# Optimization experiments

Measured on AMD Instinct MI355X. Metric: run time of the kernel, lower is better.

## Reference

```python
import jax, jax.numpy as jnp
import numpy as np

N_SRC = 50000
N_DST = 50000
N_EDGES = 1_600_000
D_IN = 128
D_OUT = 128
NUM_HEADS = 8
SCALE = float((D_OUT // NUM_HEADS) ** 0.5)


def setup_inputs() -> dict:
    key = jax.random.key(0)
    ks = jax.random.split(key, 10)
    s = 1.0 / np.sqrt(D_IN)
    return {
        "src_feat": jax.random.normal(ks[0], (N_SRC, D_IN), dtype=jnp.float32),
        "dst_feat": jax.random.normal(ks[1], (N_DST, D_OUT), dtype=jnp.float32),
        "src_idx": jax.random.randint(ks[2], (N_EDGES,), 0, N_SRC, dtype=jnp.int64),
        "dst_idx": jax.random.randint(ks[3], (N_EDGES,), 0, N_DST, dtype=jnp.int64),
        "Wq": jax.random.normal(ks[4], (D_OUT, D_OUT), dtype=jnp.float32) * s,
        "bq": jnp.zeros((D_OUT,), dtype=jnp.float32),
        "Wk": jax.random.normal(ks[5], (D_OUT, D_IN), dtype=jnp.float32) * s,
        "bk": jnp.zeros((D_OUT,), dtype=jnp.float32),
        "Wv": jax.random.normal(ks[6], (D_OUT, D_IN), dtype=jnp.float32) * s,
        "bv": jnp.zeros((D_OUT,), dtype=jnp.float32),
    }


def reference(src_feat, dst_feat, src_idx, dst_idx, Wq, bq, Wk, bk, Wv, bv):
    # Node-level projections (torch Linear: x @ W.T + b)
    Q = dst_feat @ Wq.T + bq            # [N_dst, D_OUT]
    K = src_feat @ Wk.T + bk            # [N_src, D_OUT]
    V = src_feat @ Wv.T + bv            # [N_src, D_OUT]

    # Edge-wise full-dim dot-product score (heads only affect the scale)
    score = jnp.sum(Q[dst_idx] * K[src_idx], axis=-1) / SCALE  # [E]

    # Segment softmax over incoming edges of each destination node
    m = jax.ops.segment_max(score, dst_idx, num_segments=N_DST)   # [N_dst]
    e = jnp.exp(score - m[dst_idx])                               # [E]
    denom = jax.ops.segment_sum(e, dst_idx, num_segments=N_DST)   # [N_dst]
    attn = e / denom[dst_idx]                                     # [E]

    # Weighted V scatter-sum to destination nodes
    out = jax.ops.segment_sum(attn[:, None] * V[src_idx], dst_idx,
                              num_segments=N_DST)                 # [N_dst, D_OUT]
    return out
```

## Files before the change

kernel.cpp:

```cpp
#include <hip/hip_runtime.h>
#include <hip/hip_bf16.h>


#define D 128
#define INV_SCALE 0.25f
#define E1 4096
#define BCAP 10240

typedef __attribute__((ext_vector_type(8))) short bf16x8;
typedef __attribute__((ext_vector_type(4))) float f32x4;
typedef __attribute__((ext_vector_type(4))) int v4i;
typedef __attribute__((ext_vector_type(4))) unsigned v4u;

static __device__ __forceinline__ unsigned short f2bf(float f) {
  unsigned u = __float_as_uint(f);
  u += 0x7fff + ((u >> 16) & 1);
  return (unsigned short)(u >> 16);
}
static __device__ __forceinline__ float bfl(unsigned u) {
  return __uint_as_float(u << 16);
}
static __device__ __forceinline__ float bfh(unsigned u) {
  return __uint_as_float(u & 0xffff0000u);
}

__global__ __launch_bounds__(256) void cvt_w_kernel(
    const float* __restrict__ Wq, const float* __restrict__ Wk,
    const float* __restrict__ Wv, unsigned short* __restrict__ oq,
    unsigned short* __restrict__ ok, unsigned short* __restrict__ ov, int n) {
  int i = blockIdx.x * 256 + threadIdx.x;
  if (i < n) {
    oq[i] = f2bf(Wq[i]);
    ok[i] = f2bf(Wk[i]);
    ov[i] = f2bf(Wv[i]);
  }
}

__global__ __launch_bounds__(256) void gemm_q_kernel(
    const float* __restrict__ X, const unsigned short* __restrict__ Wb,
    const float* __restrict__ bias, float* __restrict__ out, int N) {
  const int lane = threadIdx.x & 63;
  const int l15 = lane & 15, quad = lane >> 4;
  const int row0 = blockIdx.x * 64 + (threadIdx.x >> 6) * 16;

  f32x4 acc[8];
#pragma unroll
  for (int t = 0; t < 8; ++t) acc[t] = (f32x4){0.f, 0.f, 0.f, 0.f};

  int ar = row0 + l15;
  if (ar >= N) ar = N - 1;
  const float* ap = X + (size_t)ar * D + quad * 8;

#pragma unroll
  for (int kc = 0; kc < 4; ++kc) {
    float4 a0 = *(const float4*)(ap + kc * 32);
    float4 a1 = *(const float4*)(ap + kc * 32 + 4);
    bf16x8 a;
    a[0] = f2bf(a0.x); a[1] = f2bf(a0.y); a[2] = f2bf(a0.z); a[3] = f2bf(a0.w);
    a[4] = f2bf(a1.x); a[5] = f2bf(a1.y); a[6] = f2bf(a1.z); a[7] = f2bf(a1.w);
#pragma unroll
    for (int t = 0; t < 8; ++t) {
      bf16x8 b =
          *(const bf16x8*)(Wb + (size_t)(t * 16 + l15) * D + kc * 32 + quad * 8);
      acc[t] = __builtin_amdgcn_mfma_f32_16x16x32_bf16(a, b, acc[t], 0, 0, 0);
    }
  }
#pragma unroll
  for (int t = 0; t < 8; ++t) {
    const int c = t * 16 + l15;
    const float bc = bias[c];
#pragma unroll
    for (int r = 0; r < 4; ++r) {
      const int row = row0 + quad * 4 + r;
      if (row < N) out[(size_t)row * D + c] = acc[t][r] + bc;
    }
  }
}

__global__ __launch_bounds__(256) void gemm_kv_kernel(
    const float* __restrict__ X, const unsigned short* __restrict__ Wk,
    const float* __restrict__ bk, const unsigned short* __restrict__ Wv,
    const float* __restrict__ bv, unsigned short* __restrict__ KV, int N) {
  __shared__ unsigned short stage[64][256];
  const int tid = threadIdx.x;
  const int lane = tid & 63;
  const int l15 = lane & 15, quad = lane >> 4;
  const int wave = tid >> 6;
  const int row0 = blockIdx.x * 64 + wave * 16;

  f32x4 accK[8], accV[8];
#pragma unroll
  for (int t = 0; t < 8; ++t) {
    accK[t] = (f32x4){0.f, 0.f, 0.f, 0.f};
    accV[t] = (f32x4){0.f, 0.f, 0.f, 0.f};
  }

  int ar = row0 + l15;
  if (ar >= N) ar = N - 1;
  const float* ap = X + (size_t)ar * D + quad * 8;

#pragma unroll
  for (int kc = 0; kc < 4; ++kc) {
    float4 a0 = *(const float4*)(ap + kc * 32);
    float4 a1 = *(const float4*)(ap + kc * 32 + 4);
    bf16x8 a;
    a[0] = f2bf(a0.x); a[1] = f2bf(a0.y); a[2] = f2bf(a0.z); a[3] = f2bf(a0.w);
    a[4] = f2bf(a1.x); a[5] = f2bf(a1.y); a[6] = f2bf(a1.z); a[7] = f2bf(a1.w);
#pragma unroll
    for (int t = 0; t < 8; ++t) {
      const size_t boff = (size_t)(t * 16 + l15) * D + kc * 32 + quad * 8;
      bf16x8 b0 = *(const bf16x8*)(Wk + boff);
      bf16x8 b1 = *(const bf16x8*)(Wv + boff);
      accK[t] = __builtin_amdgcn_mfma_f32_16x16x32_bf16(a, b0, accK[t], 0, 0, 0);
      accV[t] = __builtin_amdgcn_mfma_f32_16x16x32_bf16(a, b1, accV[t], 0, 0, 0);
    }
  }
#pragma unroll
  for (int t = 0; t < 8; ++t) {
    const int c = t * 16 + l15;
    const float bkc = bk[c], bvc = bv[c];
    const int ki = ((c >> 2) << 3) + (c & 3);
#pragma unroll
    for (int r = 0; r < 4; ++r) {
      const int lr = wave * 16 + quad * 4 + r;
      stage[lr][ki] = f2bf(accK[t][r] + bkc);
      stage[lr][ki + 4] = f2bf(accV[t][r] + bvc);
    }
  }
  __syncthreads();
  const int row_base = blockIdx.x * 64;
#pragma unroll
  for (int i = 0; i < 8; ++i) {
    int idx = i * 256 + tid;
    int lr = idx >> 5;
    int c8 = (idx & 31) << 3;
    int grow = row_base + lr;
    if (grow < N)
      *(f32x4*)(KV + (size_t)grow * 256 + c8) = *(const f32x4*)&stage[lr][c8];
  }
}

__global__ __launch_bounds__(256) void bin1_kernel(
    const int* __restrict__ src_idx, const int* __restrict__ dst_idx,
    int* __restrict__ bins, int* __restrict__ bcount, int n) {
  __shared__ int h[256], basebuf[256], cur[256];
  const int tid = threadIdx.x;
  const int e0 = blockIdx.x * E1;
  int dv[16], sv[16];
#pragma unroll
  for (int i = 0; i < 4; ++i) {
    int e = e0 + i * 1024 + tid * 4;
    if (e + 3 < n) {
      v4i d4 = __builtin_nontemporal_load((const v4i*)(dst_idx + e));
      v4i s4 = __builtin_nontemporal_load((const v4i*)(src_idx + e));
      dv[4 * i + 0] = d4.x; dv[4 * i + 1] = d4.y;
      dv[4 * i + 2] = d4.z; dv[4 * i + 3] = d4.w;
      sv[4 * i + 0] = s4.x; sv[4 * i + 1] = s4.y;
      sv[4 * i + 2] = s4.z; sv[4 * i + 3] = s4.w;
    } else {
      for (int k = 0; k < 4; ++k) {
        int ee = e + k;
        dv[4 * i + k] = (ee < n) ? dst_idx[ee] : -1;
        sv[4 * i + k] = (ee < n) ? src_idx[ee] : 0;
      }
    }
  }
  h[tid] = 0;
  __syncthreads();
#pragma unroll
  for (int i = 0; i < 16; ++i)
    if (dv[i] >= 0) atomicAdd(&h[dv[i] >> 8], 1);
  __syncthreads();
  const int c = h[tid];
  if (c > 0) basebuf[tid] = tid * BCAP + atomicAdd(&bcount[tid], c);
  cur[tid] = 0;
  __syncthreads();
#pragma unroll
  for (int i = 0; i < 16; ++i) {
    if (dv[i] >= 0) {
      const int b = dv[i] >> 8;
      const int r = atomicAdd(&cur[b], 1);
      const int off = basebuf[b] + r;
      if (off < (b + 1) * BCAP)
        bins[off] = sv[i] | ((dv[i] & 255) << 17);
    }
  }
}

__global__ __launch_bounds__(256) void bin2_kernel(
    const int* __restrict__ bins, const int* __restrict__ bcount,
    int* __restrict__ csr, int* __restrict__ rowptr, int n_dst, int n_edges) {
  __shared__ int h[256], ofs[256], cur[256], red[256];
  const int tid = threadIdx.x;
  const int b = blockIdx.x;
  red[tid] = (tid < b) ? min(bcount[tid], BCAP) : 0;
  __syncthreads();
  for (int off = 128; off > 0; off >>= 1) {
    if (tid < off) red[tid] += red[tid + off];
    __syncthreads();
  }
  const int gbase = red[0];
  const int cnt = min(bcount[b], BCAP);
  h[tid] = 0;
  __syncthreads();
  const int* bb = bins + b * BCAP;
  for (int i = tid; i < cnt; i += 256) atomicAdd(&h[(bb[i] >> 17) & 255], 1);
  __syncthreads();
  const int myh = h[tid];
  red[tid] = myh;
  __syncthreads();
  for (int off = 1; off < 256; off <<= 1) {
    int t = (tid >= off) ? red[tid - off] : 0;
    __syncthreads();
    red[tid] += t;
    __syncthreads();
  }
  ofs[tid] = red[tid] - myh;
  cur[tid] = 0;
  const int d = b * 256 + tid;
  if (d < n_dst) rowptr[d] = gbase + ofs[tid];
  if (b == 0 && tid == 0) rowptr[n_dst] = n_edges;
  __syncthreads();
  for (int i = tid; i < cnt; i += 256) {
    const int p = bb[i];
    const int j = (p >> 17) & 255;
    const int r = atomicAdd(&cur[j], 1);
    csr[gbase + ofs[j] + r] = p & 0x1ffff;
  }
}

__global__ __launch_bounds__(256) void fused_agg_kernel(
    const float* __restrict__ Q, const unsigned short* __restrict__ KV,
    const int* __restrict__ csr, const int* __restrict__ rowptr,
    float* __restrict__ out, int n_dst) {
  const int lane = threadIdx.x & 63;
  const int half = lane >> 5;
  const int hl = lane & 31;
  int d = blockIdx.x * 4 + (threadIdx.x >> 6);
  if (d >= n_dst) return;
  d = __builtin_amdgcn_readfirstlane(d);
  const int start = __builtin_amdgcn_readfirstlane(rowptr[d]);
  const int n = __builtin_amdgcn_readfirstlane(rowptr[d + 1]) - start;

  float4 q = *(const float4*)(Q + (size_t)d * D + 4 * hl);
  q.x *= INV_SCALE; q.y *= INV_SCALE; q.z *= INV_SCALE; q.w *= INV_SCALE;

  float4 acc = make_float4(0.f, 0.f, 0.f, 0.f);
  float den = 0.f;

  for (int base = 0; base < n; base += 64) {
    const int il = base + lane;
    const int iv =
        __builtin_nontemporal_load(csr + start + ((il < n) ? il : (n - 1)));
    const int m = min(64, n - base);
    for (int j8 = 0; j8 < m; j8 += 8) {
      float pv[4];
      v4u kv[4];
      bool val[4];
#pragma unroll
      for (int u = 0; u < 4; ++u) {
        const int jj = j8 + 2 * u + half;
        val[u] = jj < m;
        const int s = __shfl(iv, jj, 64);
        kv[u] = *(const v4u*)(KV + (size_t)s * 256 + hl * 8);
        pv[u] = q.x * bfl(kv[u].x) + q.y * bfh(kv[u].x) + q.z * bfl(kv[u].y) +
                q.w * bfh(kv[u].y);
      }
#pragma unroll
      for (int u = 0; u < 4; ++u) {
        float p = pv[u];
#pragma unroll
        for (int msk = 16; msk > 0; msk >>= 1) p += __shfl_xor(p, msk, 64);
        const float e = val[u] ? __expf(p) : 0.f;
        acc.x += e * bfl(kv[u].z);
        acc.y += e * bfh(kv[u].z);
        acc.z += e * bfl(kv[u].w);
        acc.w += e * bfh(kv[u].w);
        den += e;
      }
    }
  }

  acc.x += __shfl_xor(acc.x, 32, 64);
  acc.y += __shfl_xor(acc.y, 32, 64);
  acc.z += __shfl_xor(acc.z, 32, 64);
  acc.w += __shfl_xor(acc.w, 32, 64);
  den += __shfl_xor(den, 32, 64);

  if (half == 0) {
    const float r = (n > 0) ? 1.0f / den : 0.f;
    f32x4 o = (f32x4){acc.x * r, acc.y * r, acc.z * r, acc.w * r};
    __builtin_nontemporal_store(o, (f32x4*)(out + (size_t)d * D + 4 * hl));
  }
}

extern "C" void kernel_launch(void* const* d_in, const int* in_sizes, int n_in,
                              void* d_out, int out_size, void* d_ws,
                              size_t ws_size, hipStream_t stream) {
  const float* src_feat = (const float*)d_in[0];
  const float* dst_feat = (const float*)d_in[1];
  const int* src_idx = (const int*)d_in[2];
  const int* dst_idx = (const int*)d_in[3];
  const float* Wq = (const float*)d_in[4];
  const float* bq = (const float*)d_in[5];
  const float* Wk = (const float*)d_in[6];
  const float* bk = (const float*)d_in[7];
  const float* Wv = (const float*)d_in[8];
  const float* bv = (const float*)d_in[9];

  const int n_src = in_sizes[0] / D;
  const int n_dst = in_sizes[1] / D;
  const int n_edges = in_sizes[2];
  const int nbk = (n_dst + 255) >> 8;

  float* out = (float*)d_out;

  float* Q = (float*)d_ws;
  unsigned short* KV = (unsigned short*)(Q + (size_t)n_dst * D);
  unsigned short* Wqb = KV + (size_t)n_src * 256;
  unsigned short* Wkb = Wqb + D * D;
  unsigned short* Wvb = Wkb + D * D;
  int* bcount = (int*)(Wvb + D * D);
  int* rowptr = bcount + 256;
  int* csr = rowptr + (n_dst + 1);
  int* bins = csr + n_edges;

  (void)hipMemsetAsync(bcount, 0, 256 * sizeof(int), stream);

  dim3 blk(256);

  cvt_w_kernel<<<dim3((D * D + 255) / 256), blk, 0, stream>>>(
      Wq, Wk, Wv, Wqb, Wkb, Wvb, D * D);
  gemm_q_kernel<<<dim3((n_dst + 63) / 64), blk, 0, stream>>>(dst_feat, Wqb, bq,
                                                             Q, n_dst);
  gemm_kv_kernel<<<dim3((n_src + 63) / 64), blk, 0, stream>>>(
      src_feat, Wkb, bk, Wvb, bv, KV, n_src);

  bin1_kernel<<<dim3((n_edges + E1 - 1) / E1), blk, 0, stream>>>(
      src_idx, dst_idx, bins, bcount, n_edges);
  bin2_kernel<<<dim3(nbk), blk, 0, stream>>>(bins, bcount, csr, rowptr, n_dst,
                                             n_edges);

  fused_agg_kernel<<<dim3((n_dst + 3) / 4), blk, 0, stream>>>(Q, KV, csr,
                                                              rowptr, out,
                                                              n_dst);
}
```

Measured before the change: 312.3 us.

## Merge Q/KV GEMMs into one launch and refine edge binning to 64-node buckets

Folds the Q projection and the K/V projection into a single kernel launch, with the block index choosing the branch, to remove one launch and let the two run concurrently. The CSR build moves from 256-node buckets to 1024 buckets of 64 nodes. bin1 now sorts its edges locally in shared memory before writing them out, so global bin writes become contiguous runs per bucket, and bin2 blocks are smaller with a 64-entry histogram and scan, giving more parallelism. The trade-offs are heavier shared-memory use in bin1, more bcount atomics, and a tighter per-bucket capacity of 2560 that could overflow on skewed inputs.

Result: slower. 319.2 us (+2.2%).

```diff
diff --git a/kernel.cpp b/kernel.cpp
--- a/kernel.cpp
+++ b/kernel.cpp
@@ -5,7 +5,8 @@
 #define D 128
 #define INV_SCALE 0.25f
 #define E1 4096
-#define BCAP 10240
+#define BSH 6
+#define BCAP 2560
 
 typedef __attribute__((ext_vector_type(8))) short bf16x8;
 typedef __attribute__((ext_vector_type(4))) float f32x4;
@@ -36,21 +37,65 @@
   }
 }
 
-__global__ __launch_bounds__(256) void gemm_q_kernel(
-    const float* __restrict__ X, const unsigned short* __restrict__ Wb,
-    const float* __restrict__ bias, float* __restrict__ out, int N) {
-  const int lane = threadIdx.x & 63;
+__global__ __launch_bounds__(256) void gemm_qkv_kernel(
+    const float* __restrict__ dst_feat, const float* __restrict__ src_feat,
+    const unsigned short* __restrict__ Wqb, const float* __restrict__ bq,
+    const unsigned short* __restrict__ Wkb, const float* __restrict__ bk,
+    const unsigned short* __restrict__ Wvb, const float* __restrict__ bv,
+    float* __restrict__ Q, unsigned short* __restrict__ KV, int n_dst,
+    int n_src, int gq) {
+  __shared__ unsigned short stage[64][256];
+  const int tid = threadIdx.x;
+  const int lane = tid & 63;
   const int l15 = lane & 15, quad = lane >> 4;
-  const int row0 = blockIdx.x * 64 + (threadIdx.x >> 6) * 16;
-
-  f32x4 acc[8];
-#pragma unroll
-  for (int t = 0; t < 8; ++t) acc[t] = (f32x4){0.f, 0.f, 0.f, 0.f};
-
+  const int wave = tid >> 6;
+
+  if ((int)blockIdx.x < gq) {
+    const int row0 = blockIdx.x * 64 + wave * 16;
+    f32x4 acc[8];
+#pragma unroll
+    for (int t = 0; t < 8; ++t) acc[t] = (f32x4){0.f, 0.f, 0.f, 0.f};
+    int ar = row0 + l15;
+    if (ar >= n_dst) ar = n_dst - 1;
+    const float* ap = dst_feat + (size_t)ar * D + quad * 8;
+#pragma unroll
+    for (int kc = 0; kc < 4; ++kc) {
+      float4 a0 = *(const float4*)(ap + kc * 32);
+      float4 a1 = *(const float4*)(ap + kc * 32 + 4);
+      bf16x8 a;
+      a[0] = f2bf(a0.x); a[1] = f2bf(a0.y); a[2] = f2bf(a0.z); a[3] = f2bf(a0.w);
+      a[4] = f2bf(a1.x); a[5] = f2bf(a1.y); a[6] = f2bf(a1.z); a[7] = f2bf(a1.w);
+#pragma unroll
+      for (int t = 0; t < 8; ++t) {
+        bf16x8 b = *(const bf16x8*)(Wqb + (size_t)(t * 16 + l15) * D + kc * 32 +
+                                    quad * 8);
+        acc[t] = __builtin_amdgcn_mfma_f32_16x16x32_bf16(a, b, acc[t], 0, 0, 0);
+      }
+    }
+#pragma unroll
+    for (int t = 0; t < 8; ++t) {
+      const int c = t * 16 + l15;
+      const float bc = bq[c];
+#pragma unroll
+      for (int r = 0; r < 4; ++r) {
+        const int row = row0 + quad * 4 + r;
+        if (row < n_dst) Q[(size_t)row * D + c] = acc[t][r] + bc;
+      }
+    }
+    return;
+  }
+
+  const int bb = blockIdx.x - gq;
+  const int row0 = bb * 64 + wave * 16;
+  f32x4 accK[8], accV[8];
+#pragma unroll
+  for (int t = 0; t < 8; ++t) {
+    accK[t] = (f32x4){0.f, 0.f, 0.f, 0.f};
+    accV[t] = (f32x4){0.f, 0.f, 0.f, 0.f};
+  }
   int ar = row0 + l15;
-  if (ar >= N) ar = N - 1;
-  const float* ap = X + (size_t)ar * D + quad * 8;
-
+  if (ar >= n_src) ar = n_src - 1;
+  const float* ap = src_feat + (size_t)ar * D + quad * 8;
 #pragma unroll
   for (int kc = 0; kc < 4; ++kc) {
     float4 a0 = *(const float4*)(ap + kc * 32);
@@ -60,57 +105,9 @@
     a[4] = f2bf(a1.x); a[5] = f2bf(a1.y); a[6] = f2bf(a1.z); a[7] = f2bf(a1.w);
 #pragma unroll
     for (int t = 0; t < 8; ++t) {
-      bf16x8 b =
-          *(const bf16x8*)(Wb + (size_t)(t * 16 + l15) * D + kc * 32 + quad * 8);
-      acc[t] = __builtin_amdgcn_mfma_f32_16x16x32_bf16(a, b, acc[t], 0, 0, 0);
-    }
-  }
-#pragma unroll
-  for (int t = 0; t < 8; ++t) {
-    const int c = t * 16 + l15;
-    const float bc = bias[c];
-#pragma unroll
-    for (int r = 0; r < 4; ++r) {
-      const int row = row0 + quad * 4 + r;
-      if (row < N) out[(size_t)row * D + c] = acc[t][r] + bc;
-    }
-  }
-}
-
-__global__ __launch_bounds__(256) void gemm_kv_kernel(
-    const float* __restrict__ X, const unsigned short* __restrict__ Wk,
-    const float* __restrict__ bk, const unsigned short* __restrict__ Wv,
-    const float* __restrict__ bv, unsigned short* __restrict__ KV, int N) {
-  __shared__ unsigned short stage[64][256];
-  const int tid = threadIdx.x;
-  const int lane = tid & 63;
-  const int l15 = lane & 15, quad = lane >> 4;
-  const int wave = tid >> 6;
-  const int row0 = blockIdx.x * 64 + wave * 16;
-
-  f32x4 accK[8], accV[8];
-#pragma unroll
-  for (int t = 0; t < 8; ++t) {
-    accK[t] = (f32x4){0.f, 0.f, 0.f, 0.f};
-    accV[t] = (f32x4){0.f, 0.f, 0.f, 0.f};
-  }
-
-  int ar = row0 + l15;
-  if (ar >= N) ar = N - 1;
-  const float* ap = X + (size_t)ar * D + quad * 8;
-
-#pragma unroll
-  for (int kc = 0; kc < 4; ++kc) {
-    float4 a0 = *(const float4*)(ap + kc * 32);
-    float4 a1 = *(const float4*)(ap + kc * 32 + 4);
-    bf16x8 a;
-    a[0] = f2bf(a0.x); a[1] = f2bf(a0.y); a[2] = f2bf(a0.z); a[3] = f2bf(a0.w);
-    a[4] = f2bf(a1.x); a[5] = f2bf(a1.y); a[6] = f2bf(a1.z); a[7] = f2bf(a1.w);
-#pragma unroll
-    for (int t = 0; t < 8; ++t) {
       const size_t boff = (size_t)(t * 16 + l15) * D + kc * 32 + quad * 8;
-      bf16x8 b0 = *(const bf16x8*)(Wk + boff);
-      bf16x8 b1 = *(const bf16x8*)(Wv + boff);
+      bf16x8 b0 = *(const bf16x8*)(Wkb + boff);
+      bf16x8 b1 = *(const bf16x8*)(Wvb + boff);
       accK[t] = __builtin_amdgcn_mfma_f32_16x16x32_bf16(a, b0, accK[t], 0, 0, 0);
       accV[t] = __builtin_amdgcn_mfma_f32_16x16x32_bf16(a, b1, accV[t], 0, 0, 0);
     }
@@ -128,14 +125,14 @@
     }
   }
   __syncthreads();
-  const int row_base = blockIdx.x * 64;
+  const int row_base = bb * 64;
 #pragma unroll
   for (int i = 0; i < 8; ++i) {
     int idx = i * 256 + tid;
     int lr = idx >> 5;
     int c8 = (idx & 31) << 3;
     int grow = row_base + lr;
-    if (grow < N)
+    if (grow < n_src)
       *(f32x4*)(KV + (size_t)grow * 256 + c8) = *(const f32x4*)&stage[lr][c8];
   }
 }
@@ -143,9 +140,16 @@
 __global__ __launch_bounds__(256) void bin1_kernel(
     const int* __restrict__ src_idx, const int* __restrict__ dst_idx,
     int* __restrict__ bins, int* __restrict__ bcount, int n) {
-  __shared__ int h[256], basebuf[256], cur[256];
+  __shared__ int h[1024];
+  __shared__ int lofs[1024];
+  __shared__ int base[1024];
+  __shared__ int scan[256];
+  __shared__ int entries[E1];
+  __shared__ unsigned short bkt[E1];
   const int tid = threadIdx.x;
   const int e0 = blockIdx.x * E1;
+  const int cnt = min(E1, n - e0);
+
   int dv[16], sv[16];
 #pragma unroll
   for (int i = 0; i < 4; ++i) {
@@ -165,35 +169,67 @@
       }
     }
   }
-  h[tid] = 0;
+  h[tid] = 0; h[tid + 256] = 0; h[tid + 512] = 0; h[tid + 768] = 0;
   __syncthreads();
 #pragma unroll
   for (int i = 0; i < 16; ++i)
-    if (dv[i] >= 0) atomicAdd(&h[dv[i] >> 8], 1);
-  __syncthreads();
-  const int c = h[tid];
-  if (c > 0) basebuf[tid] = tid * BCAP + atomicAdd(&bcount[tid], c);
-  cur[tid] = 0;
+    if (dv[i] >= 0) atomicAdd(&h[dv[i] >> BSH], 1);
+  __syncthreads();
+  int s0 = h[4 * tid], s1 = h[4 * tid + 1], s2 = h[4 * tid + 2],
+      s3 = h[4 * tid + 3];
+  const int tsum = s0 + s1 + s2 + s3;
+  scan[tid] = tsum;
+  __syncthreads();
+  for (int off = 1; off < 256; off <<= 1) {
+    int t = (tid >= off) ? scan[tid - off] : 0;
+    __syncthreads();
+    scan[tid] += t;
+    __syncthreads();
+  }
+  const int ex = scan[tid] - tsum;
+  lofs[4 * tid + 0] = ex;
+  lofs[4 * tid + 1] = ex + s0;
+  lofs[4 * tid + 2] = ex + s0 + s1;
+  lofs[4 * tid + 3] = ex + s0 + s1 + s2;
+  {
+    int hs[4] = {s0, s1, s2, s3};
+#pragma unroll
+    for (int j = 0; j < 4; ++j) {
+      const int b = 4 * tid + j;
+      if (hs[j] > 0) base[b] = b * BCAP + atomicAdd(&bcount[b], hs[j]);
+    }
+  }
+  __syncthreads();
+  h[4 * tid] = lofs[4 * tid]; h[4 * tid + 1] = lofs[4 * tid + 1];
+  h[4 * tid + 2] = lofs[4 * tid + 2]; h[4 * tid + 3] = lofs[4 * tid + 3];
   __syncthreads();
 #pragma unroll
   for (int i = 0; i < 16; ++i) {
     if (dv[i] >= 0) {
-      const int b = dv[i] >> 8;
-      const int r = atomicAdd(&cur[b], 1);
-      const int off = basebuf[b] + r;
-      if (off < (b + 1) * BCAP)
-        bins[off] = sv[i] | ((dv[i] & 255) << 17);
-    }
+      const int b = dv[i] >> BSH;
+      const int p = atomicAdd(&h[b], 1);
+      entries[p] = sv[i] | ((dv[i] & 63) << 17);
+      bkt[p] = (unsigned short)b;
+    }
+  }
+  __syncthreads();
+  for (int p = tid; p < cnt; p += 256) {
+    const int b = bkt[p];
+    const int g = base[b] + (p - lofs[b]);
+    if (g < (b + 1) * BCAP)
+      __builtin_nontemporal_store(entries[p], bins + g);
   }
 }
 
 __global__ __launch_bounds__(256) void bin2_kernel(
     const int* __restrict__ bins, const int* __restrict__ bcount,
     int* __restrict__ csr, int* __restrict__ rowptr, int n_dst, int n_edges) {
-  __shared__ int h[256], ofs[256], cur[256], red[256];
+  __shared__ int h[64], ofs[64], cur[64], red[256];
   const int tid = threadIdx.x;
   const int b = blockIdx.x;
-  red[tid] = (tid < b) ? min(bcount[tid], BCAP) : 0;
+  int part = 0;
+  for (int j = tid; j < b; j += 256) part += min(bcount[j], BCAP);
+  red[tid] = part;
   __syncthreads();
   for (int off = 128; off > 0; off >>= 1) {
     if (tid < off) red[tid] += red[tid + off];
@@ -201,29 +237,30 @@
   }
   const int gbase = red[0];
   const int cnt = min(bcount[b], BCAP);
-  h[tid] = 0;
+  if (tid < 64) h[tid] = 0;
   __syncthreads();
   const int* bb = bins + b * BCAP;
-  for (int i = tid; i < cnt; i += 256) atomicAdd(&h[(bb[i] >> 17) & 255], 1);
-  __syncthreads();
-  const int myh = h[tid];
-  red[tid] = myh;
-  __syncthreads();
-  for (int off = 1; off < 256; off <<= 1) {
-    int t = (tid >= off) ? red[tid - off] : 0;
-    __syncthreads();
-    red[tid] += t;
-    __syncthreads();
-  }
-  ofs[tid] = red[tid] - myh;
-  cur[tid] = 0;
-  const int d = b * 256 + tid;
-  if (d < n_dst) rowptr[d] = gbase + ofs[tid];
+  for (int i = tid; i < cnt; i += 256) atomicAdd(&h[(bb[i] >> 17) & 63], 1);
+  __syncthreads();
+  if (tid < 64) red[tid] = h[tid];
+  __syncthreads();
+  for (int off = 1; off < 64; off <<= 1) {
+    int t = (tid >= off && tid < 64) ? red[tid - off] : 0;
+    __syncthreads();
+    if (tid < 64) red[tid] += t;
+    __syncthreads();
+  }
+  if (tid < 64) {
+    ofs[tid] = red[tid] - h[tid];
+    cur[tid] = 0;
+    const int d = b * 64 + tid;
+    if (d < n_dst) rowptr[d] = gbase + ofs[tid];
+  }
   if (b == 0 && tid == 0) rowptr[n_dst] = n_edges;
   __syncthreads();
   for (int i = tid; i < cnt; i += 256) {
     const int p = bb[i];
-    const int j = (p >> 17) & 255;
+    const int j = (p >> 17) & 63;
     const int r = atomicAdd(&cur[j], 1);
     csr[gbase + ofs[j] + r] = p & 0x1ffff;
   }
@@ -311,7 +348,7 @@
   const int n_src = in_sizes[0] / D;
   const int n_dst = in_sizes[1] / D;
   const int n_edges = in_sizes[2];
-  const int nbk = (n_dst + 255) >> 8;
+  const int nbk = (n_dst + 63) >> BSH;
 
   float* out = (float*)d_out;
 
@@ -321,20 +358,20 @@
   unsigned short* Wkb = Wqb + D * D;
   unsigned short* Wvb = Wkb + D * D;
   int* bcount = (int*)(Wvb + D * D);
-  int* rowptr = bcount + 256;
+  int* rowptr = bcount + 1024;
   int* csr = rowptr + (n_dst + 1);
   int* bins = csr + n_edges;
 
-  (void)hipMemsetAsync(bcount, 0, 256 * sizeof(int), stream);
+  (void)hipMemsetAsync(bcount, 0, 1024 * sizeof(int), stream);
 
   dim3 blk(256);
 
   cvt_w_kernel<<<dim3((D * D + 255) / 256), blk, 0, stream>>>(
       Wq, Wk, Wv, Wqb, Wkb, Wvb, D * D);
-  gemm_q_kernel<<<dim3((n_dst + 63) / 64), blk, 0, stream>>>(dst_feat, Wqb, bq,
-                                                             Q, n_dst);
-  gemm_kv_kernel<<<dim3((n_src + 63) / 64), blk, 0, stream>>>(
-      src_feat, Wkb, bk, Wvb, bv, KV, n_src);
+  const int gq = (n_dst + 63) / 64;
+  const int gkv = (n_src + 63) / 64;
+  gemm_qkv_kernel<<<dim3(gq + gkv), blk, 0, stream>>>(
+      dst_feat, src_feat, Wqb, bq, Wkb, bk, Wvb, bv, Q, KV, n_dst, n_src, gq);
 
   bin1_kernel<<<dim3((n_edges + E1 - 1) / E1), blk, 0, stream>>>(
       src_idx, dst_idx, bins, bcount, n_edges);
```
